# Optimization experiments

Measured on AMD Instinct MI355X. Metric: run time of the kernel, lower is better.

## Reference

```python
import jax, jax.numpy as jnp
import numpy as np

# module hyper-parameters (VoronoiDecoder defaults)
S = 256          # n_seeds
Q = 262144       # query uv points
EPS = 1e-8
W_MIN = 0.005
BETA = 0.02
RAW_TEMP = 5.0
H_MIN, H_MAX = 0.5, 2.0
J_BETA_SCALE = 1.0
J_WIDTH_BONUS = 0.15
J_KEFF_K0 = 3.0
J_KEFF_S = 0.35
J_TRIPLE_LAMBDA = 0.15
J_TRIPLE_POWER = 1.5
KNN_K = 8
SOFTMIN_TAU = 0.002


def setup_inputs() -> dict:
    key = jax.random.key(0)
    ks = jax.random.split(key, 7)
    return {
        "uv": jax.random.uniform(ks[0], (Q, 2), jnp.float32),
        "seeds_raw": jax.random.uniform(ks[1], (S, 2), jnp.float32),
        "w_raw": jax.random.normal(ks[2], (S, S), jnp.float32),
        "h_raw": jax.random.normal(ks[3], (S,), jnp.float32),
        "theta": jax.random.normal(ks[4], (S,), jnp.float32),
        "a_raw": 0.3 * jax.random.normal(ks[5], (S,), jnp.float32),
        "seed_gates": jax.random.normal(ks[6], (S,), jnp.float32),
    }


def reference(uv, seeds_raw, w_raw, h_raw, theta, a_raw, seed_gates):
    seeds = seeds_raw  # seeds_uv is identity

    # --- pairwise seed distances (default buffers: all faces non-periodic,
    # seed_face_id all zero -> periodic wrap is a no-op -> plain euclidean) ---
    pd = jnp.linalg.norm(seeds[None, :, :] - seeds[:, None, :], axis=-1)  # (S,S)
    w_max_pair = jnp.maximum(0.8 * pd, W_MIN + EPS)
    w_geo = W_MIN + (w_max_pair - W_MIN) * jax.nn.sigmoid(w_raw / RAW_TEMP)
    W = 0.5 * (w_geo + w_geo.T)  # symmetric pairwise wall widths (S,S)

    h = H_MIN + (H_MAX - H_MIN) * jax.nn.sigmoid(h_raw)  # (S,) heights
    gates = jax.nn.sigmoid(seed_gates)                    # (S,) seed gates

    # --- anisotropic (unit-determinant) metric distance per seed ---
    c, sn = jnp.cos(theta), jnp.sin(theta)
    sc = jnp.exp(a_raw)  # anisotropy scale per seed
    dx = uv[:, None, 0] - seeds[None, :, 0]  # (Q,S)
    dy = uv[:, None, 1] - seeds[None, :, 1]
    xp = (c * dx + sn * dy) / sc   # rotate into seed frame, scale axes
    yp = (-sn * dx + c * dy) * sc
    d = jnp.sqrt(xp * xp + yp * yp + EPS)  # (Q,S) metric distances

    # --- kNN over seeds ---
    negk, idx = jax.lax.top_k(-d, KNN_K)   # (Q,K)
    dk = -negk
    d1, d3 = dk[:, 0], dk[:, 2]
    i1, i2 = idx[:, 0], idx[:, 1]
    w_pair = W[i1, i2]  # width of the wall between the 2 nearest cells

    # --- junction effects via softmin cell-membership weights ---
    p = jax.nn.softmax(-d / (BETA * J_BETA_SCALE), axis=-1)  # (Q,S)
    k_eff = 1.0 / (jnp.sum(p * p, axis=-1) + EPS)            # effective #cells
    bonus = J_WIDTH_BONUS * jax.nn.sigmoid((k_eff - J_KEFF_K0) / J_KEFF_S)
    triple = J_TRIPLE_LAMBDA * jnp.exp(-((d3 - d1) / (w_pair + EPS)) ** J_TRIPLE_POWER)
    w_eff = w_pair * (1.0 + bonus + triple)

    # --- softmin distance to Voronoi boundary over kNN bisectors ---
    b = 0.5 * (dk[:, 1:] - d1[:, None])  # (Q,K-1) bisector half-gaps
    sdist = -SOFTMIN_TAU * jax.nn.logsumexp(-b / SOFTMIN_TAU, axis=-1)
    wall = jax.nn.sigmoid((0.5 * w_eff - sdist) / BETA)  # shell occupancy

    h_blend = p @ h        # (Q,) blended height
    g_blend = p @ gates    # (Q,) blended gate
    return wall * g_blend * h_blend
```

## Files before the change

kernel.cpp:

```cpp
#include <hip/hip_runtime.h>

#define NSEED 256

typedef float v2f __attribute__((ext_vector_type(2)));
typedef float v4f __attribute__((ext_vector_type(4)));

__device__ __forceinline__ float fast_exp(float x) {
  return __builtin_amdgcn_exp2f(x * 1.4426950408889634f);
}
__device__ __forceinline__ float sigf(float x) {
  return 1.0f / (1.0f + fast_exp(-x));
}
__device__ __forceinline__ float med3(float x, float lo, float hi) {
  return __builtin_amdgcn_fmed3f(x, lo, hi);
}
__device__ __forceinline__ v2f vfma(v2f a, v2f b, v2f c) {
  return __builtin_elementwise_fma(a, b, c);
}

__global__ __launch_bounds__(256) void voronoi_kernel(
    const float* __restrict__ uv, const float* __restrict__ seeds,
    const float* __restrict__ w_raw, const float* __restrict__ h_raw,
    const float* __restrict__ theta, const float* __restrict__ a_raw,
    const float* __restrict__ seed_gates, float* __restrict__ out, int nq) {
  __shared__ v4f Pp[(NSEED / 2) * 4];

  {
    int s = threadIdx.x;
    float sx = seeds[2 * s], sy = seeds[2 * s + 1];
    float th = theta[s];
    float c = cosf(th), sn = sinf(th);
    float sc = expf(a_raw[s]);
    float inv = 1.0f / sc;
    float h = 0.5f + 1.5f * sigf(h_raw[s]);
    float g = sigf(seed_gates[s]);
    float* base = (float*)&Pp[(s >> 1) * 4];
    int b = s & 1;
    base[0 + b] = sx;
    base[2 + b] = sy;
    base[4 + b] = c * inv;
    base[6 + b] = sn * inv;
    base[8 + b] = -sn * sc;
    base[10 + b] = c * sc;
    base[12 + b] = h;
    base[14 + b] = g;
  }
  __syncthreads();

  const int q = blockIdx.x * 256 + threadIdx.x;
  if (q >= nq) return;
  const float2 uvq = ((const float2*)uv)[q];
  const float u = uvq.x, v = uvq.y;
  const v2f uu = {u, u}, vv = {v, v};
  const v2f eps2 = {1e-8f, 1e-8f};

  float dk0 = 3e38f, dk1 = 3e38f, dk2 = 3e38f, dk3 = 3e38f;
  float dk4 = 3e38f, dk5 = 3e38f, dk6 = 3e38f, dk7 = 3e38f;
  int i0 = 0, i1 = 0;

#define INSERT(dval, sidx)                  \
  {                                         \
    float _d = (dval);                      \
    bool c0 = _d < dk0;                     \
    bool c1 = _d < dk1;                     \
    int sh = c0 ? i0 : (sidx);              \
    i1 = c1 ? sh : i1;                      \
    i0 = c0 ? (sidx) : i0;                  \
    dk7 = med3(_d, dk6, dk7);               \
    dk6 = med3(_d, dk5, dk6);               \
    dk5 = med3(_d, dk4, dk5);               \
    dk4 = med3(_d, dk3, dk4);               \
    dk3 = med3(_d, dk2, dk3);               \
    dk2 = med3(_d, dk1, dk2);               \
    dk1 = med3(_d, dk0, dk1);               \
    dk0 = fminf(_d, dk0);                   \
  }

#pragma unroll 4
  for (int p = 0; p < NSEED / 2; ++p) {
    v4f q0 = Pp[4 * p + 0];
    v4f q1 = Pp[4 * p + 1];
    v4f q2 = Pp[4 * p + 2];
    v2f dx = uu - q0.xy, dy = vv - q0.zw;
    v2f xp = vfma(q1.xy, dx, q1.zw * dy);
    v2f yp = vfma(q2.xy, dx, q2.zw * dy);
    v2f d2 = vfma(xp, xp, vfma(yp, yp, eps2));
    INSERT(d2.x, 2 * p);
    INSERT(d2.y, 2 * p + 1);
  }
#undef INSERT

  dk0 = __builtin_amdgcn_sqrtf(dk0);
  dk1 = __builtin_amdgcn_sqrtf(dk1);
  dk2 = __builtin_amdgcn_sqrtf(dk2);
  dk3 = __builtin_amdgcn_sqrtf(dk3);
  dk4 = __builtin_amdgcn_sqrtf(dk4);
  dk5 = __builtin_amdgcn_sqrtf(dk5);
  dk6 = __builtin_amdgcn_sqrtf(dk6);
  dk7 = __builtin_amdgcn_sqrtf(dk7);

  const float d1 = dk0, d3 = dk2;

  const float KB = 72.13475204444817f;
  const float C1 = d1 * KB;
  v2f S1 = {0.f, 0.f}, S2 = {0.f, 0.f}, Sh = {0.f, 0.f}, Sg = {0.f, 0.f};
#pragma unroll 4
  for (int p = 0; p < NSEED / 2; ++p) {
    v4f q0 = Pp[4 * p + 0];
    v4f q1 = Pp[4 * p + 1];
    v4f q2 = Pp[4 * p + 2];
    v4f q3 = Pp[4 * p + 3];
    v2f dx = uu - q0.xy, dy = vv - q0.zw;
    v2f xp = vfma(q1.xy, dx, q1.zw * dy);
    v2f yp = vfma(q2.xy, dx, q2.zw * dy);
    v2f d2 = vfma(xp, xp, vfma(yp, yp, eps2));
    float da = __builtin_amdgcn_sqrtf(d2.x);
    float db = __builtin_amdgcn_sqrtf(d2.y);
    v2f e;
    e.x = __builtin_amdgcn_exp2f(fmaf(-KB, da, C1));
    e.y = __builtin_amdgcn_exp2f(fmaf(-KB, db, C1));
    S1 += e;
    S2 = vfma(e, e, S2);
    Sh = vfma(e, q3.xy, Sh);
    Sg = vfma(e, q3.zw, Sg);
  }
  float S1s = S1.x + S1.y;
  float S2s = S2.x + S2.y;
  float Shs = Sh.x + Sh.y;
  float Sgs = Sg.x + Sg.y;

  float ax = seeds[2 * i0], ay = seeds[2 * i0 + 1];
  float bx = seeds[2 * i1], by = seeds[2 * i1 + 1];
  float pdx = ax - bx, pdy = ay - by;
  float pd = __builtin_amdgcn_sqrtf(fmaf(pdx, pdx, pdy * pdy));
  float wmax = fmaxf(0.8f * pd, 0.005f + 1e-8f);
  float wr01 = w_raw[(i0 << 8) + i1];
  float wr10 = w_raw[(i1 << 8) + i0];
  float w_pair = 0.005f + (wmax - 0.005f) * 0.5f * (sigf(wr01 * 0.2f) + sigf(wr10 * 0.2f));

  float s1sq = S1s * S1s;
  float keff = s1sq / fmaf(1e-8f, s1sq, S2s);
  float bonus = 0.15f * sigf((keff - 3.0f) * (1.0f / 0.35f));

  float t = (d3 - d1) / (w_pair + 1e-8f);
  float t15 = t * __builtin_amdgcn_sqrtf(t);
  float triple = 0.15f * fast_exp(-t15);

  float w_eff = w_pair * (1.0f + bonus + triple);

  const float HT = 360.6737602222409f;
  float acc = 1.0f;
  acc += __builtin_amdgcn_exp2f((dk1 - dk2) * HT);
  acc += __builtin_amdgcn_exp2f((dk1 - dk3) * HT);
  acc += __builtin_amdgcn_exp2f((dk1 - dk4) * HT);
  acc += __builtin_amdgcn_exp2f((dk1 - dk5) * HT);
  acc += __builtin_amdgcn_exp2f((dk1 - dk6) * HT);
  acc += __builtin_amdgcn_exp2f((dk1 - dk7) * HT);
  float b1 = 0.5f * (dk1 - d1);
  float sdist = b1 - 0.002f * 0.6931471805599453f * __builtin_amdgcn_logf(acc);

  float wall = sigf((0.5f * w_eff - sdist) * 50.0f);
  float invS1 = 1.0f / S1s;
  out[q] = wall * (Sgs * invS1) * (Shs * invS1);
}

extern "C" void kernel_launch(void* const* d_in, const int* in_sizes, int n_in,
                              void* d_out, int out_size, void* d_ws, size_t ws_size,
                              hipStream_t stream) {
  (void)in_sizes;
  (void)n_in;
  (void)d_ws;
  (void)ws_size;
  const float* uv = (const float*)d_in[0];
  const float* seeds = (const float*)d_in[1];
  const float* w_raw = (const float*)d_in[2];
  const float* h_raw = (const float*)d_in[3];
  const float* theta = (const float*)d_in[4];
  const float* a_raw = (const float*)d_in[5];
  const float* gates = (const float*)d_in[6];
  float* out = (float*)d_out;

  int nq = out_size;
  int grid = (nq + 255) / 256;
  voronoi_kernel<<<grid, 256, 0, stream>>>(uv, seeds, w_raw, h_raw, theta,
                                           a_raw, gates, out, nq);
}
```

Baseline: 124.8 us.

## Fuse kNN and softmax passes, split seeds across two lanes per query

Merges the top-k selection pass and the softmax-sum pass into a single loop over seeds, so each distance is computed once instead of twice. The exponential no longer subtracts the nearest distance, which makes a single pass possible. Each query is now handled by two adjacent lanes, each covering half the seeds. Their top-8 lists are merged with xor shuffles and a bitonic min/sort network, and their partial sums are combined the same way. The cost is an extra shuffle-and-merge epilogue, a grid with twice as many threads, and a risk that the unshifted exponentials, and especially their squares in the sum-of-squares term, underflow when a query is far from every seed.

```diff
diff --git a/kernel.cpp b/kernel.cpp
--- a/kernel.cpp
+++ b/kernel.cpp
@@ -47,65 +47,42 @@
   }
   __syncthreads();
 
-  const int q = blockIdx.x * 256 + threadIdx.x;
+  const int t = blockIdx.x * 256 + threadIdx.x;
+  const int q = t >> 1;
+  const int par = t & 1;
   if (q >= nq) return;
   const float2 uvq = ((const float2*)uv)[q];
-  const float u = uvq.x, v = uvq.y;
-  const v2f uu = {u, u}, vv = {v, v};
+  const v2f uu = {uvq.x, uvq.x}, vv = {uvq.y, uvq.y};
   const v2f eps2 = {1e-8f, 1e-8f};
+  const float NK = -72.13475204444817f;
 
   float dk0 = 3e38f, dk1 = 3e38f, dk2 = 3e38f, dk3 = 3e38f;
   float dk4 = 3e38f, dk5 = 3e38f, dk6 = 3e38f, dk7 = 3e38f;
   int i0 = 0, i1 = 0;
-
-#define INSERT(dval, sidx)                  \
-  {                                         \
-    float _d = (dval);                      \
-    bool c0 = _d < dk0;                     \
-    bool c1 = _d < dk1;                     \
-    int sh = c0 ? i0 : (sidx);              \
-    i1 = c1 ? sh : i1;                      \
-    i0 = c0 ? (sidx) : i0;                  \
-    dk7 = med3(_d, dk6, dk7);               \
-    dk6 = med3(_d, dk5, dk6);               \
-    dk5 = med3(_d, dk4, dk5);               \
-    dk4 = med3(_d, dk3, dk4);               \
-    dk3 = med3(_d, dk2, dk3);               \
-    dk2 = med3(_d, dk1, dk2);               \
-    dk1 = med3(_d, dk0, dk1);               \
-    dk0 = fminf(_d, dk0);                   \
-  }
-
+  v2f S1 = {0.f, 0.f}, S2 = {0.f, 0.f}, Sh = {0.f, 0.f}, Sg = {0.f, 0.f};
+
+#define INS(x, sidx)             \
+  {                              \
+    float _d = (x);              \
+    bool c0 = _d < dk0;          \
+    bool c1 = _d < dk1;          \
+    int sh = c0 ? i0 : (sidx);   \
+    i1 = c1 ? sh : i1;           \
+    i0 = c0 ? (sidx) : i0;       \
+    dk7 = med3(_d, dk6, dk7);    \
+    dk6 = med3(_d, dk5, dk6);    \
+    dk5 = med3(_d, dk4, dk5);    \
+    dk4 = med3(_d, dk3, dk4);    \
+    dk3 = med3(_d, dk2, dk3);    \
+    dk2 = med3(_d, dk1, dk2);    \
+    dk1 = med3(_d, dk0, dk1);    \
+    dk0 = fminf(_d, dk0);        \
+  }
+
+  const int pbase = par * 64;
 #pragma unroll 4
-  for (int p = 0; p < NSEED / 2; ++p) {
-    v4f q0 = Pp[4 * p + 0];
-    v4f q1 = Pp[4 * p + 1];
-    v4f q2 = Pp[4 * p + 2];
-    v2f dx = uu - q0.xy, dy = vv - q0.zw;
-    v2f xp = vfma(q1.xy, dx, q1.zw * dy);
-    v2f yp = vfma(q2.xy, dx, q2.zw * dy);
-    v2f d2 = vfma(xp, xp, vfma(yp, yp, eps2));
-    INSERT(d2.x, 2 * p);
-    INSERT(d2.y, 2 * p + 1);
-  }
-#undef INSERT
-
-  dk0 = __builtin_amdgcn_sqrtf(dk0);
-  dk1 = __builtin_amdgcn_sqrtf(dk1);
-  dk2 = __builtin_amdgcn_sqrtf(dk2);
-  dk3 = __builtin_amdgcn_sqrtf(dk3);
-  dk4 = __builtin_amdgcn_sqrtf(dk4);
-  dk5 = __builtin_amdgcn_sqrtf(dk5);
-  dk6 = __builtin_amdgcn_sqrtf(dk6);
-  dk7 = __builtin_amdgcn_sqrtf(dk7);
-
-  const float d1 = dk0, d3 = dk2;
-
-  const float KB = 72.13475204444817f;
-  const float C1 = d1 * KB;
-  v2f S1 = {0.f, 0.f}, S2 = {0.f, 0.f}, Sh = {0.f, 0.f}, Sg = {0.f, 0.f};
-#pragma unroll 4
-  for (int p = 0; p < NSEED / 2; ++p) {
+  for (int k = 0; k < 64; ++k) {
+    int p = pbase + k;
     v4f q0 = Pp[4 * p + 0];
     v4f q1 = Pp[4 * p + 1];
     v4f q2 = Pp[4 * p + 2];
@@ -114,36 +91,83 @@
     v2f xp = vfma(q1.xy, dx, q1.zw * dy);
     v2f yp = vfma(q2.xy, dx, q2.zw * dy);
     v2f d2 = vfma(xp, xp, vfma(yp, yp, eps2));
+    INS(d2.x, 2 * p);
+    INS(d2.y, 2 * p + 1);
     float da = __builtin_amdgcn_sqrtf(d2.x);
     float db = __builtin_amdgcn_sqrtf(d2.y);
     v2f e;
-    e.x = __builtin_amdgcn_exp2f(fmaf(-KB, da, C1));
-    e.y = __builtin_amdgcn_exp2f(fmaf(-KB, db, C1));
+    e.x = __builtin_amdgcn_exp2f(da * NK);
+    e.y = __builtin_amdgcn_exp2f(db * NK);
     S1 += e;
     S2 = vfma(e, e, S2);
     Sh = vfma(e, q3.xy, Sh);
     Sg = vfma(e, q3.zw, Sg);
   }
+#undef INS
+
+  float b0 = __shfl_xor(dk0, 1), b1 = __shfl_xor(dk1, 1);
+  float b2 = __shfl_xor(dk2, 1), b3 = __shfl_xor(dk3, 1);
+  float b4 = __shfl_xor(dk4, 1), b5 = __shfl_xor(dk5, 1);
+  float b6 = __shfl_xor(dk6, 1), b7 = __shfl_xor(dk7, 1);
+  int j0 = __shfl_xor(i0, 1), j1 = __shfl_xor(i1, 1);
+  bool aw = b0 < dk0;
+  int I0 = aw ? j0 : i0;
+  float ec1 = aw ? dk0 : dk1;
+  int ic1 = aw ? i0 : i1;
+  float ec2 = aw ? b1 : b0;
+  int ic2 = aw ? j1 : j0;
+  int I1 = (ec2 < ec1) ? ic2 : ic1;
+
+  float m0 = fminf(dk0, b7), m1 = fminf(dk1, b6);
+  float m2 = fminf(dk2, b5), m3 = fminf(dk3, b4);
+  float m4 = fminf(dk4, b3), m5 = fminf(dk5, b2);
+  float m6 = fminf(dk6, b1), m7 = fminf(dk7, b0);
+#define CE(a, b)             \
+  {                          \
+    float _lo = fminf(a, b); \
+    float _hi = fmaxf(a, b); \
+    a = _lo;                 \
+    b = _hi;                 \
+  }
+  CE(m0, m4) CE(m1, m5) CE(m2, m6) CE(m3, m7)
+  CE(m0, m2) CE(m1, m3) CE(m4, m6) CE(m5, m7)
+  CE(m0, m1) CE(m2, m3) CE(m4, m5) CE(m6, m7)
+#undef CE
+
+  dk0 = __builtin_amdgcn_sqrtf(m0);
+  dk1 = __builtin_amdgcn_sqrtf(m1);
+  dk2 = __builtin_amdgcn_sqrtf(m2);
+  dk3 = __builtin_amdgcn_sqrtf(m3);
+  dk4 = __builtin_amdgcn_sqrtf(m4);
+  dk5 = __builtin_amdgcn_sqrtf(m5);
+  dk6 = __builtin_amdgcn_sqrtf(m6);
+  dk7 = __builtin_amdgcn_sqrtf(m7);
+  const float d1 = dk0, d3 = dk2;
+
   float S1s = S1.x + S1.y;
   float S2s = S2.x + S2.y;
   float Shs = Sh.x + Sh.y;
   float Sgs = Sg.x + Sg.y;
-
-  float ax = seeds[2 * i0], ay = seeds[2 * i0 + 1];
-  float bx = seeds[2 * i1], by = seeds[2 * i1 + 1];
+  S1s += __shfl_xor(S1s, 1);
+  S2s += __shfl_xor(S2s, 1);
+  Shs += __shfl_xor(Shs, 1);
+  Sgs += __shfl_xor(Sgs, 1);
+
+  float ax = seeds[2 * I0], ay = seeds[2 * I0 + 1];
+  float bx = seeds[2 * I1], by = seeds[2 * I1 + 1];
   float pdx = ax - bx, pdy = ay - by;
   float pd = __builtin_amdgcn_sqrtf(fmaf(pdx, pdx, pdy * pdy));
   float wmax = fmaxf(0.8f * pd, 0.005f + 1e-8f);
-  float wr01 = w_raw[(i0 << 8) + i1];
-  float wr10 = w_raw[(i1 << 8) + i0];
+  float wr01 = w_raw[(I0 << 8) + I1];
+  float wr10 = w_raw[(I1 << 8) + I0];
   float w_pair = 0.005f + (wmax - 0.005f) * 0.5f * (sigf(wr01 * 0.2f) + sigf(wr10 * 0.2f));
 
   float s1sq = S1s * S1s;
   float keff = s1sq / fmaf(1e-8f, s1sq, S2s);
   float bonus = 0.15f * sigf((keff - 3.0f) * (1.0f / 0.35f));
 
-  float t = (d3 - d1) / (w_pair + 1e-8f);
-  float t15 = t * __builtin_amdgcn_sqrtf(t);
+  float tt = (d3 - d1) / (w_pair + 1e-8f);
+  float t15 = tt * __builtin_amdgcn_sqrtf(tt);
   float triple = 0.15f * fast_exp(-t15);
 
   float w_eff = w_pair * (1.0f + bonus + triple);
@@ -156,12 +180,12 @@
   acc += __builtin_amdgcn_exp2f((dk1 - dk5) * HT);
   acc += __builtin_amdgcn_exp2f((dk1 - dk6) * HT);
   acc += __builtin_amdgcn_exp2f((dk1 - dk7) * HT);
-  float b1 = 0.5f * (dk1 - d1);
-  float sdist = b1 - 0.002f * 0.6931471805599453f * __builtin_amdgcn_logf(acc);
+  float b1s = 0.5f * (dk1 - d1);
+  float sdist = b1s - 0.002f * 0.6931471805599453f * __builtin_amdgcn_logf(acc);
 
   float wall = sigf((0.5f * w_eff - sdist) * 50.0f);
   float invS1 = 1.0f / S1s;
-  out[q] = wall * (Sgs * invS1) * (Shs * invS1);
+  if (par == 0) out[q] = wall * (Sgs * invS1) * (Shs * invS1);
 }
 
 extern "C" void kernel_launch(void* const* d_in, const int* in_sizes, int n_in,
@@ -181,7 +205,8 @@
   float* out = (float*)d_out;
 
   int nq = out_size;
-  int grid = (nq + 255) / 256;
+  long long threads = 2LL * nq;
+  int grid = (int)((threads + 255) / 256);
   voronoi_kernel<<<grid, 256, 0, stream>>>(uv, seeds, w_raw, h_raw, theta,
                                            a_raw, gates, out, nq);
 }
```

Measured after the change: 116.4 us. 6.8% less time.

## Fuse kNN and softmax passes into one loop, precompute seed params in separate kernel

Applied to the files above, without the earlier changes.

The two passes over all seeds (kNN selection, then softmax accumulation) become a single loop. To allow this, the exponentials are no longer shifted by the nearest distance d1, since d1 is unknown until the loop ends. The per-seed transform now runs once in a small setup kernel that writes to the workspace. The main kernel then reads those parameters from global memory with uniform loads instead of from LDS. This halves the distance computation and removes the per-block setup and barrier, at the cost of an extra launch and reduced numerical headroom: exp2 of the unshifted distances can underflow for queries far from every seed.

```diff
diff --git a/kernel.cpp b/kernel.cpp
--- a/kernel.cpp
+++ b/kernel.cpp
@@ -18,77 +18,91 @@
   return __builtin_elementwise_fma(a, b, c);
 }
 
+__global__ void seed_setup_kernel(const float* __restrict__ seeds,
+                                  const float* __restrict__ h_raw,
+                                  const float* __restrict__ theta,
+                                  const float* __restrict__ a_raw,
+                                  const float* __restrict__ seed_gates,
+                                  float* __restrict__ Pg) {
+  int s = threadIdx.x;
+  if (s >= NSEED) return;
+  float sx = seeds[2 * s], sy = seeds[2 * s + 1];
+  float th = theta[s];
+  float c = cosf(th), sn = sinf(th);
+  float sc = expf(a_raw[s]);
+  float inv = 1.0f / sc;
+  float h = 0.5f + 1.5f * sigf(h_raw[s]);
+  float g = sigf(seed_gates[s]);
+  float* base = Pg + (s >> 1) * 16;
+  int b = s & 1;
+  base[0 + b] = sx;
+  base[2 + b] = sy;
+  base[4 + b] = c * inv;
+  base[6 + b] = sn * inv;
+  base[8 + b] = -sn * sc;
+  base[10 + b] = c * sc;
+  base[12 + b] = h;
+  base[14 + b] = g;
+}
+
 __global__ __launch_bounds__(256) void voronoi_kernel(
     const float* __restrict__ uv, const float* __restrict__ seeds,
-    const float* __restrict__ w_raw, const float* __restrict__ h_raw,
-    const float* __restrict__ theta, const float* __restrict__ a_raw,
-    const float* __restrict__ seed_gates, float* __restrict__ out, int nq) {
-  __shared__ v4f Pp[(NSEED / 2) * 4];
-
-  {
-    int s = threadIdx.x;
-    float sx = seeds[2 * s], sy = seeds[2 * s + 1];
-    float th = theta[s];
-    float c = cosf(th), sn = sinf(th);
-    float sc = expf(a_raw[s]);
-    float inv = 1.0f / sc;
-    float h = 0.5f + 1.5f * sigf(h_raw[s]);
-    float g = sigf(seed_gates[s]);
-    float* base = (float*)&Pp[(s >> 1) * 4];
-    int b = s & 1;
-    base[0 + b] = sx;
-    base[2 + b] = sy;
-    base[4 + b] = c * inv;
-    base[6 + b] = sn * inv;
-    base[8 + b] = -sn * sc;
-    base[10 + b] = c * sc;
-    base[12 + b] = h;
-    base[14 + b] = g;
-  }
-  __syncthreads();
-
+    const float* __restrict__ w_raw, const float* __restrict__ Pg,
+    float* __restrict__ out, int nq) {
   const int q = blockIdx.x * 256 + threadIdx.x;
   if (q >= nq) return;
   const float2 uvq = ((const float2*)uv)[q];
-  const float u = uvq.x, v = uvq.y;
-  const v2f uu = {u, u}, vv = {v, v};
+  const v2f uu = {uvq.x, uvq.x}, vv = {uvq.y, uvq.y};
   const v2f eps2 = {1e-8f, 1e-8f};
+  const float NK = -72.13475204444817f;
 
   float dk0 = 3e38f, dk1 = 3e38f, dk2 = 3e38f, dk3 = 3e38f;
   float dk4 = 3e38f, dk5 = 3e38f, dk6 = 3e38f, dk7 = 3e38f;
   int i0 = 0, i1 = 0;
+  v2f S1 = {0.f, 0.f}, S2 = {0.f, 0.f}, Sh = {0.f, 0.f}, Sg = {0.f, 0.f};
 
-#define INSERT(dval, sidx)                  \
-  {                                         \
-    float _d = (dval);                      \
-    bool c0 = _d < dk0;                     \
-    bool c1 = _d < dk1;                     \
-    int sh = c0 ? i0 : (sidx);              \
-    i1 = c1 ? sh : i1;                      \
-    i0 = c0 ? (sidx) : i0;                  \
-    dk7 = med3(_d, dk6, dk7);               \
-    dk6 = med3(_d, dk5, dk6);               \
-    dk5 = med3(_d, dk4, dk5);               \
-    dk4 = med3(_d, dk3, dk4);               \
-    dk3 = med3(_d, dk2, dk3);               \
-    dk2 = med3(_d, dk1, dk2);               \
-    dk1 = med3(_d, dk0, dk1);               \
-    dk0 = fminf(_d, dk0);                   \
+#define INS(x, sidx)             \
+  {                              \
+    float _d = (x);              \
+    bool c0 = _d < dk0;          \
+    bool c1 = _d < dk1;          \
+    int sh = c0 ? i0 : (sidx);   \
+    i1 = c1 ? sh : i1;           \
+    i0 = c0 ? (sidx) : i0;       \
+    dk7 = med3(_d, dk6, dk7);    \
+    dk6 = med3(_d, dk5, dk6);    \
+    dk5 = med3(_d, dk4, dk5);    \
+    dk4 = med3(_d, dk3, dk4);    \
+    dk3 = med3(_d, dk2, dk3);    \
+    dk2 = med3(_d, dk1, dk2);    \
+    dk1 = med3(_d, dk0, dk1);    \
+    dk0 = fminf(_d, dk0);        \
   }
 
-#pragma unroll 4
-  for (int p = 0; p < NSEED / 2; ++p) {
-    v4f q0 = Pp[4 * p + 0];
-    v4f q1 = Pp[4 * p + 1];
-    v4f q2 = Pp[4 * p + 2];
+  const v4f* __restrict__ PG = (const v4f*)Pg;
+#pragma unroll 8
+  for (int k = 0; k < NSEED / 2; ++k) {
+    v4f q0 = PG[4 * k + 0];
+    v4f q1 = PG[4 * k + 1];
+    v4f q2 = PG[4 * k + 2];
+    v4f q3 = PG[4 * k + 3];
     v2f dx = uu - q0.xy, dy = vv - q0.zw;
     v2f xp = vfma(q1.xy, dx, q1.zw * dy);
     v2f yp = vfma(q2.xy, dx, q2.zw * dy);
     v2f d2 = vfma(xp, xp, vfma(yp, yp, eps2));
-    INSERT(d2.x, 2 * p);
-    INSERT(d2.y, 2 * p + 1);
+    INS(d2.x, 2 * k);
+    INS(d2.y, 2 * k + 1);
+    float da = __builtin_amdgcn_sqrtf(d2.x);
+    float db = __builtin_amdgcn_sqrtf(d2.y);
+    v2f e;
+    e.x = __builtin_amdgcn_exp2f(da * NK);
+    e.y = __builtin_amdgcn_exp2f(db * NK);
+    S1 += e;
+    S2 = vfma(e, e, S2);
+    Sh = vfma(e, q3.xy, Sh);
+    Sg = vfma(e, q3.zw, Sg);
   }
-#undef INSERT
+#undef INS
 
   dk0 = __builtin_amdgcn_sqrtf(dk0);
   dk1 = __builtin_amdgcn_sqrtf(dk1);
@@ -98,32 +112,8 @@
   dk5 = __builtin_amdgcn_sqrtf(dk5);
   dk6 = __builtin_amdgcn_sqrtf(dk6);
   dk7 = __builtin_amdgcn_sqrtf(dk7);
-
   const float d1 = dk0, d3 = dk2;
 
-  const float KB = 72.13475204444817f;
-  const float C1 = d1 * KB;
-  v2f S1 = {0.f, 0.f}, S2 = {0.f, 0.f}, Sh = {0.f, 0.f}, Sg = {0.f, 0.f};
-#pragma unroll 4
-  for (int p = 0; p < NSEED / 2; ++p) {
-    v4f q0 = Pp[4 * p + 0];
-    v4f q1 = Pp[4 * p + 1];
-    v4f q2 = Pp[4 * p + 2];
-    v4f q3 = Pp[4 * p + 3];
-    v2f dx = uu - q0.xy, dy = vv - q0.zw;
-    v2f xp = vfma(q1.xy, dx, q1.zw * dy);
-    v2f yp = vfma(q2.xy, dx, q2.zw * dy);
-    v2f d2 = vfma(xp, xp, vfma(yp, yp, eps2));
-    float da = __builtin_amdgcn_sqrtf(d2.x);
-    float db = __builtin_amdgcn_sqrtf(d2.y);
-    v2f e;
-    e.x = __builtin_amdgcn_exp2f(fmaf(-KB, da, C1));
-    e.y = __builtin_amdgcn_exp2f(fmaf(-KB, db, C1));
-    S1 += e;
-    S2 = vfma(e, e, S2);
-    Sh = vfma(e, q3.xy, Sh);
-    Sg = vfma(e, q3.zw, Sg);
-  }
   float S1s = S1.x + S1.y;
   float S2s = S2.x + S2.y;
   float Shs = Sh.x + Sh.y;
@@ -142,8 +132,8 @@
   float keff = s1sq / fmaf(1e-8f, s1sq, S2s);
   float bonus = 0.15f * sigf((keff - 3.0f) * (1.0f / 0.35f));
 
-  float t = (d3 - d1) / (w_pair + 1e-8f);
-  float t15 = t * __builtin_amdgcn_sqrtf(t);
+  float tt = (d3 - d1) / (w_pair + 1e-8f);
+  float t15 = tt * __builtin_amdgcn_sqrtf(tt);
   float triple = 0.15f * fast_exp(-t15);
 
   float w_eff = w_pair * (1.0f + bonus + triple);
@@ -156,8 +146,8 @@
   acc += __builtin_amdgcn_exp2f((dk1 - dk5) * HT);
   acc += __builtin_amdgcn_exp2f((dk1 - dk6) * HT);
   acc += __builtin_amdgcn_exp2f((dk1 - dk7) * HT);
-  float b1 = 0.5f * (dk1 - d1);
-  float sdist = b1 - 0.002f * 0.6931471805599453f * __builtin_amdgcn_logf(acc);
+  float b1s = 0.5f * (dk1 - d1);
+  float sdist = b1s - 0.002f * 0.6931471805599453f * __builtin_amdgcn_logf(acc);
 
   float wall = sigf((0.5f * w_eff - sdist) * 50.0f);
   float invS1 = 1.0f / S1s;
@@ -169,7 +159,6 @@
                               hipStream_t stream) {
   (void)in_sizes;
   (void)n_in;
-  (void)d_ws;
   (void)ws_size;
   const float* uv = (const float*)d_in[0];
   const float* seeds = (const float*)d_in[1];
@@ -179,9 +168,10 @@
   const float* a_raw = (const float*)d_in[5];
   const float* gates = (const float*)d_in[6];
   float* out = (float*)d_out;
+  float* Pg = (float*)d_ws;
 
+  seed_setup_kernel<<<1, 256, 0, stream>>>(seeds, h_raw, theta, a_raw, gates, Pg);
   int nq = out_size;
   int grid = (nq + 255) / 256;
-  voronoi_kernel<<<grid, 256, 0, stream>>>(uv, seeds, w_raw, h_raw, theta,
-                                           a_raw, gates, out, nq);
+  voronoi_kernel<<<grid, 256, 0, stream>>>(uv, seeds, w_raw, Pg, out, nq);
 }
```

New measurement: 114.6 us. 1.09x faster.
